# Kernel tuning notes

Hardware: AMD Instinct MI355X
Metric: run time of the kernel (lower is better)

The kernel has to match this reference:

```python
import jax, jax.numpy as jnp
import numpy as np
from jax import lax

B_, T_, C_ = 8, 1024, 768
H_, W_ = 32, 32
N_LAYER, LAYER_ID = 12, 5


def _fancy_init():
    # faithful 'fancy' init from Random_SpatialMix._init_weights
    r01 = LAYER_ID / (N_LAYER - 1)
    r1a0 = 1.0 - LAYER_ID / N_LAYER
    h = np.arange(C_, dtype=np.float64)
    decay = -5 + 8 * (h / (C_ - 1)) ** (0.7 + 1.3 * r01)
    zig = ((np.arange(C_) + 1) % 3 - 1) * 0.5
    first = np.log(0.3) + zig
    xlin = h / C_
    mix_k = xlin ** r1a0
    mix_v = xlin ** r1a0 + 0.3 * r01
    mix_r = xlin ** (0.5 * r1a0)
    f32 = lambda a: jnp.asarray(a, jnp.float32)
    return f32(decay), f32(first), f32(mix_k), f32(mix_v), f32(mix_r)


def setup_inputs() -> dict:
    key = jax.random.key(0)
    ks = jax.random.split(key, 6)
    s = 1.0 / np.sqrt(C_)
    x = jax.random.normal(ks[0], (B_, T_, C_), jnp.float32)
    Wk = jax.random.normal(ks[1], (C_, C_), jnp.float32) * s
    Wv = jax.random.normal(ks[2], (C_, C_), jnp.float32) * s
    Wr = jax.random.normal(ks[3], (C_, C_), jnp.float32) * s
    Wo = jax.random.normal(ks[4], (C_, C_), jnp.float32) * s
    decay, first, mk, mv, mr = _fancy_init()
    perm = jax.random.permutation(ks[5], C_).astype(jnp.int32)
    return dict(x=x, w_key=Wk, w_value=Wv, w_receptance=Wr, w_output=Wo,
                spatial_decay=decay, spatial_first=first,
                mix_k=mk, mix_v=mv, mix_r=mr, perm=perm, H=H_, W=W_)


def _shift2d(a, dh, dw, H, W):
    # zero-padded 2D shift of [B,H,W,g]
    pad = [(0, 0), (max(dh, 0), max(-dh, 0)), (max(dw, 0), max(-dw, 0)), (0, 0)]
    a = jnp.pad(a, pad)
    return a[:, max(-dh, 0):max(-dh, 0) + H, max(-dw, 0):max(-dw, 0) + W, :]


def q_shift(x, H, W, shift_pixel=1, gamma=0.25):
    # VRWKV q_shift: 4 channel groups shifted right/left/down/up, rest copied
    B, T, C = x.shape
    xi = x.reshape(B, H, W, C)
    g = int(C * gamma)
    parts = [
        _shift2d(xi[..., 0:g], 0, shift_pixel, H, W),
        _shift2d(xi[..., g:2 * g], 0, -shift_pixel, H, W),
        _shift2d(xi[..., 2 * g:3 * g], shift_pixel, 0, H, W),
        _shift2d(xi[..., 3 * g:4 * g], -shift_pixel, 0, H, W),
        xi[..., 4 * g:],
    ]
    return jnp.concatenate(parts, axis=-1).reshape(B, T, C)


def wkv(w, u, k, v):
    # RWKV-v4 WKV kernel (numerically stable form). w,u: [C]; k,v: [B,T,C]
    w = -jnp.exp(w)  # kernel applies w = -exp(w)
    B, T, C = k.shape

    def step(carry, kv):
        a, b, p = carry  # each [B,C]
        kt, vt = kv
        q = jnp.maximum(p, u + kt)
        e1 = jnp.exp(p - q)
        e2 = jnp.exp(u + kt - q)
        y = (e1 * a + e2 * vt) / (e1 * b + e2)
        q2 = jnp.maximum(p + w, kt)
        e1 = jnp.exp(p + w - q2)
        e2 = jnp.exp(kt - q2)
        return (e1 * a + e2 * vt, e1 * b + e2, q2), y

    init = (jnp.zeros((B, C), k.dtype), jnp.zeros((B, C), k.dtype),
            jnp.full((B, C), -1e38, k.dtype))
    _, y = lax.scan(step, init, (jnp.moveaxis(k, 1, 0), jnp.moveaxis(v, 1, 0)))
    return jnp.moveaxis(y, 0, 1)


def reference(x, w_key, w_value, w_receptance, w_output,
              spatial_decay, spatial_first, mix_k, mix_v, mix_r, perm, H, W):
    B, T, C = x.shape
    xx = q_shift(x, H, W)
    xk = x * mix_k + xx * (1 - mix_k)
    xv = x * mix_v + xx * (1 - mix_v)
    xr = x * mix_r + xx * (1 - mix_r)
    k = xk @ w_key.T
    v = xv @ w_value.T
    sr = jax.nn.sigmoid(xr @ w_receptance.T)
    # training path: shuffle CHANNEL axis (RevShuffle dim=2), run WKV, reverse
    ks_ = k[:, :, perm]
    vs_ = v[:, :, perm]
    wkv_s = wkv(spatial_decay / T, spatial_first / T, ks_, vs_)
    rev = jnp.zeros_like(perm).at[perm].set(jnp.arange(C, dtype=perm.dtype))
    wkv_out = wkv_s[:, :, rev]
    return (sr * wkv_out) @ w_output.T
```

## Files before the change

kernel.cpp:

```cpp
#include <hip/hip_runtime.h>
#include <hip/hip_bf16.h>
#include <stdint.h>

#define B_N 8
#define T_N 1024
#define C_N 768
#define M_N (B_N*T_N)
#define NCH 32
#define LCH (T_N/NCH)
#define BK32 32
#define KS  (C_N/BK32)

typedef __attribute__((ext_vector_type(4))) float f32x4;
typedef __attribute__((ext_vector_type(8))) short s16x8;
typedef __attribute__((ext_vector_type(4))) unsigned short u16x4;

__device__ __forceinline__ unsigned short f2bf(float f){
  unsigned int u = __float_as_uint(f);
  u += 0x7FFFu + ((u >> 16) & 1u);
  return (unsigned short)(u >> 16);
}
__device__ __forceinline__ float bf2f(unsigned short h){
  return __uint_as_float(((unsigned int)h) << 16);
}

__device__ __forceinline__ void async16(const unsigned short* g, unsigned short* l){
  __builtin_amdgcn_global_load_lds(
      (const __attribute__((address_space(1))) unsigned int*)g,
      (__attribute__((address_space(3))) unsigned int*)l, 16, 0, 0);
}

__global__ __launch_bounds__(256) void prep_mix(
    const float* __restrict__ x,
    const float* __restrict__ Wk, const float* __restrict__ Wv,
    const float* __restrict__ Wr, const float* __restrict__ Wo,
    const int* __restrict__ perm,
    const float* __restrict__ mk, const float* __restrict__ mv, const float* __restrict__ mr,
    unsigned short* __restrict__ Wall, unsigned short* __restrict__ Wop,
    unsigned short* __restrict__ xk, unsigned short* __restrict__ xv,
    unsigned short* __restrict__ xr)
{
  if (blockIdx.x < 2304){
    int idx = blockIdx.x*256 + threadIdx.x;
    int r = idx / C_N, c = idx - r*C_N;
    int pr = perm[r];
    Wall[idx]                     = f2bf(Wk[pr*C_N + c]);
    Wall[idx +   (size_t)C_N*C_N] = f2bf(Wv[pr*C_N + c]);
    Wall[idx + 2*(size_t)C_N*C_N] = f2bf(Wr[pr*C_N + c]);
    Wop[idx] = f2bf(Wo[r*C_N + perm[c]]);
    return;
  }
  int idx = (blockIdx.x - 2304)*256 + threadIdx.x;
  int n  = idx / (C_N/4);
  int c4 = (idx - n*(C_N/4)) * 4;
  int t = n & (T_N-1);
  int h = t >> 5, w = t & 31;
  int grp = c4 / 192;
  int dh = (grp==2) ? -1 : (grp==3) ? 1 : 0;
  int dw = (grp==0) ? -1 : (grp==1) ? 1 : 0;
  int h2 = h + dh, w2 = w + dw;
  bool valid = ((unsigned)h2 < 32u) && ((unsigned)w2 < 32u);
  f32x4 xc = *(const f32x4*)(x + (size_t)n*C_N + c4);
  f32x4 xx = {0.f,0.f,0.f,0.f};
  if (valid) xx = *(const f32x4*)(x + (size_t)(n + dh*32 + dw)*C_N + c4);
  f32x4 vk = *(const f32x4*)(mk + c4);
  f32x4 vv = *(const f32x4*)(mv + c4);
  f32x4 vr = *(const f32x4*)(mr + c4);
  u16x4 ok, ov, orr;
  #pragma unroll
  for (int i=0;i<4;++i){
    float d = xc[i] - xx[i];
    ok[i]  = f2bf(xx[i] + vk[i]*d);
    ov[i]  = f2bf(xx[i] + vv[i]*d);
    orr[i] = f2bf(xx[i] + vr[i]*d);
  }
  *(u16x4*)(xk + (size_t)n*C_N + c4) = ok;
  *(u16x4*)(xv + (size_t)n*C_N + c4) = ov;
  *(u16x4*)(xr + (size_t)n*C_N + c4) = orr;
}

__global__ __launch_bounds__(256, 4) void gemm_kvr(
    const unsigned short* __restrict__ xk, const unsigned short* __restrict__ xv,
    const unsigned short* __restrict__ xr,
    const unsigned short* __restrict__ Wall,
    unsigned short* __restrict__ kb, unsigned short* __restrict__ vb,
    unsigned short* __restrict__ srb)
{
  int flat = blockIdx.y * gridDim.x + blockIdx.x;
  const int xcd = flat & 7, q = flat >> 3;
  const int mb = xcd*8 + (q & 7);
  const int nb = q >> 3;
  const int m0 = mb * 128;
  const int n0 = nb * 128;
  const int z  = nb / 6;
  const unsigned short* A = (z==0)? xk : (z==1)? xv : xr;

  __shared__ union {
    struct { unsigned short As[2][128*BK32]; unsigned short Bs[2][128*BK32]; } s;
    unsigned short ct[64*132];
  } u;
  const int tid = threadIdx.x;
  const int lane = tid & 63, wid = tid >> 6;
  const int wr = wid >> 1, wc = wid & 1;
  f32x4 acc[4][4];
  #pragma unroll
  for (int i=0;i<4;++i)
    #pragma unroll
    for (int j=0;j<4;++j) acc[i][j] = (f32x4){0.f,0.f,0.f,0.f};

  const int sgcol = ((lane & 3) ^ ((lane >> 3) & 3)) * 8;
  const int srow  = lane >> 2;
  const int lr  = lane & 15;
  const int kh  = lane >> 4;
  const int phys = (kh ^ ((lr >> 1) & 3)) * 8;

  auto stage = [&](int buf, int k0){
    #pragma unroll
    for (int i=0;i<2;++i){
      int rbase = i*64 + wid*16;
      async16(&A   [(size_t)(m0 + rbase + srow)*C_N + k0 + sgcol], &u.s.As[buf][rbase*BK32]);
      async16(&Wall[(size_t)(n0 + rbase + srow)*C_N + k0 + sgcol], &u.s.Bs[buf][rbase*BK32]);
    }
  };

  auto compute = [&](int buf){
    s16x8 af[4], bfr[4];
    #pragma unroll
    for (int mi=0;mi<4;++mi) af[mi]  = *(const s16x8*)&u.s.As[buf][(wr*64 + mi*16 + lr)*BK32 + phys];
    #pragma unroll
    for (int ni=0;ni<4;++ni) bfr[ni] = *(const s16x8*)&u.s.Bs[buf][(wc*64 + ni*16 + lr)*BK32 + phys];
    __builtin_amdgcn_s_setprio(1);
    #pragma unroll
    for (int mi=0;mi<4;++mi)
      #pragma unroll
      for (int ni=0;ni<4;++ni)
        acc[mi][ni] = __builtin_amdgcn_mfma_f32_16x16x32_bf16(af[mi], bfr[ni], acc[mi][ni], 0,0,0);
    __builtin_amdgcn_s_setprio(0);
  };

  stage(0, 0);
  #pragma unroll 1
  for (int t = 0; t < KS; ++t){
    if (t + 1 < KS){
      stage((t+1)&1, (t+1)*BK32);
      asm volatile("s_waitcnt vmcnt(4)" ::: "memory");
    } else {
      asm volatile("s_waitcnt vmcnt(0)" ::: "memory");
    }
    __builtin_amdgcn_s_barrier();
    compute(t & 1);
    __builtin_amdgcn_s_barrier();
  }

  unsigned short* dst = (z==0)? kb : (z==1)? vb : srb;
  const int colbase = n0 - z*C_N;
  const int lr4 = (lane>>4)*4, lc = lane & 15;
  #pragma unroll
  for (int p=0;p<2;++p){
    if (p) __builtin_amdgcn_s_barrier();
    if (wr == p){
      #pragma unroll
      for (int mi=0;mi<4;++mi){
        #pragma unroll
        for (int ni=0;ni<4;++ni){
          #pragma unroll
          for (int i=0;i<4;++i){
            int r  = mi*16 + lr4 + i;
            int cc = wc*64 + ni*16 + lc;
            float val = acc[mi][ni][i];
            if (z==2) val = 1.f/(1.f + __expf(-val));
            u.ct[r*132 + cc] = f2bf(val);
          }
        }
      }
    }
    __builtin_amdgcn_s_barrier();
    #pragma unroll
    for (int qq=0;qq<4;++qq){
      int f = (qq*256 + tid)*8;
      int r = f >> 7, cc = f & 127;
      s16x8 v8 = *(const s16x8*)&u.ct[r*132 + cc];
      *(s16x8*)&dst[(size_t)(m0 + p*64 + r)*C_N + colbase + cc] = v8;
    }
  }
}

__global__ __launch_bounds__(256, 4) void gemm_out(
    const unsigned short* __restrict__ A, const unsigned short* __restrict__ Bw,
    float* __restrict__ out)
{
  int flat = blockIdx.y * gridDim.x + blockIdx.x;
  const int xcd = flat & 7, q = flat >> 3;
  const int mb = xcd*8 + (q & 7);
  const int nb = q >> 3;
  const int m0 = mb*128, n0 = nb*128;
  __shared__ __align__(16) unsigned short As[2][128*BK32];
  __shared__ __align__(16) unsigned short Bs[2][128*BK32];
  const int tid = threadIdx.x;
  const int lane = tid & 63, wid = tid >> 6;
  const int wr = wid >> 1, wc = wid & 1;
  f32x4 acc[4][4];
  #pragma unroll
  for (int i=0;i<4;++i)
    #pragma unroll
    for (int j=0;j<4;++j) acc[i][j] = (f32x4){0.f,0.f,0.f,0.f};

  const int sgcol = ((lane & 3) ^ ((lane >> 3) & 3)) * 8;
  const int srow  = lane >> 2;
  const int lr  = lane & 15;
  const int kh  = lane >> 4;
  const int phys = (kh ^ ((lr >> 1) & 3)) * 8;

  auto stage = [&](int buf, int k0){
    #pragma unroll
    for (int i=0;i<2;++i){
      int rbase = i*64 + wid*16;
      async16(&A [(size_t)(m0 + rbase + srow)*C_N + k0 + sgcol], &As[buf][rbase*BK32]);
      async16(&Bw[(size_t)(n0 + rbase + srow)*C_N + k0 + sgcol], &Bs[buf][rbase*BK32]);
    }
  };

  auto compute = [&](int buf){
    s16x8 af[4], bfr[4];
    #pragma unroll
    for (int mi=0;mi<4;++mi) af[mi]  = *(const s16x8*)&As[buf][(wr*64 + mi*16 + lr)*BK32 + phys];
    #pragma unroll
    for (int ni=0;ni<4;++ni) bfr[ni] = *(const s16x8*)&Bs[buf][(wc*64 + ni*16 + lr)*BK32 + phys];
    __builtin_amdgcn_s_setprio(1);
    #pragma unroll
    for (int mi=0;mi<4;++mi)
      #pragma unroll
      for (int ni=0;ni<4;++ni)
        acc[mi][ni] = __builtin_amdgcn_mfma_f32_16x16x32_bf16(af[mi], bfr[ni], acc[mi][ni], 0,0,0);
    __builtin_amdgcn_s_setprio(0);
  };

  stage(0, 0);
  #pragma unroll 1
  for (int t = 0; t < KS; ++t){
    if (t + 1 < KS){
      stage((t+1)&1, (t+1)*BK32);
      asm volatile("s_waitcnt vmcnt(4)" ::: "memory");
    } else {
      asm volatile("s_waitcnt vmcnt(0)" ::: "memory");
    }
    __builtin_amdgcn_s_barrier();
    compute(t & 1);
    __builtin_amdgcn_s_barrier();
  }

  const int lr4 = (lane>>4)*4, lc = lane & 15;
  #pragma unroll
  for (int mi=0;mi<4;++mi)
    #pragma unroll
    for (int ni=0;ni<4;++ni)
      #pragma unroll
      for (int i=0;i<4;++i){
        int m = m0 + wr*64 + mi*16 + lr4 + i;
        int n = n0 + wc*64 + ni*16 + lc;
        out[(size_t)m*C_N + n] = acc[mi][ni][i];
      }
}

__global__ __launch_bounds__(256) void wkv_phase1(
    const unsigned short* __restrict__ kb, const unsigned short* __restrict__ vb,
    const float* __restrict__ decay,
    float* __restrict__ sa, float* __restrict__ sb, float* __restrict__ sp)
{
  int g = blockIdx.x*256 + threadIdx.x;
  int j = g % C_N;
  int cb = g / C_N;
  int b = cb % B_N, c = cb / B_N;
  float w = -__expf(decay[j] * (1.0f/T_N));
  float a = 0.f, bb = 0.f, p = -1e38f;
  size_t base = ((size_t)b*T_N + c*LCH)*C_N + j;
  #pragma unroll 4
  for (int t = 0; t < LCH; ++t){
    size_t o = base + (size_t)t*C_N;
    float kt = bf2f(kb[o]), vt = bf2f(vb[o]);
    float pw = p + w;
    float q2 = fmaxf(pw, kt);
    float e1 = __expf(pw - q2), e2 = __expf(kt - q2);
    a  = e1*a + e2*vt;
    bb = e1*bb + e2;
    p  = q2;
  }
  sa[g] = a; sb[g] = bb; sp[g] = p;
}

__global__ __launch_bounds__(256) void wkv_phase2(
    const float* __restrict__ decay,
    float* __restrict__ sa, float* __restrict__ sb, float* __restrict__ sp)
{
  int g = blockIdx.x*256 + threadIdx.x;
  int j = g % C_N, b = g / C_N;
  float w = -__expf(decay[j] * (1.0f/T_N));
  float wL = w * (float)LCH;
  float a = 0.f, bb = 0.f, p = -1e38f;
  for (int c = 0; c < NCH; ++c){
    size_t idx = ((size_t)c*B_N + b)*C_N + j;
    float la = sa[idx], lb = sb[idx], lp = sp[idx];
    sa[idx] = a; sb[idx] = bb; sp[idx] = p;
    float p1 = p + wL;
    float pn = fmaxf(p1, lp);
    float e1 = __expf(p1 - pn), e2 = __expf(lp - pn);
    a  = e1*a + e2*la;
    bb = e1*bb + e2*lb;
    p  = pn;
  }
}

__global__ __launch_bounds__(256) void wkv_phase3(
    const unsigned short* __restrict__ kb, const unsigned short* __restrict__ vb,
    const unsigned short* __restrict__ srb,
    const float* __restrict__ decay, const float* __restrict__ first,
    const float* __restrict__ sa, const float* __restrict__ sb,
    const float* __restrict__ sp,
    unsigned short* __restrict__ zp)
{
  int g = blockIdx.x*256 + threadIdx.x;
  int j = g % C_N;
  int cb = g / C_N;
  int b = cb % B_N, c = cb / B_N;
  float w = -__expf(decay[j] * (1.0f/T_N));
  float u = first[j] * (1.0f/T_N);
  float a = sa[g], bb = sb[g], p = sp[g];
  size_t base = ((size_t)b*T_N + c*LCH)*C_N + j;
  #pragma unroll 2
  for (int t = 0; t < LCH; ++t){
    size_t o = base + (size_t)t*C_N;
    float kt = bf2f(kb[o]), vt = bf2f(vb[o]);
    float uk = u + kt;
    float q  = fmaxf(p, uk);
    float e1 = __expf(p - q), e2 = __expf(uk - q);
    float y  = __fdividef(e1*a + e2*vt, e1*bb + e2);
    zp[o] = f2bf(bf2f(srb[o]) * y);
    float pw = p + w;
    float q2 = fmaxf(pw, kt);
    float e1b = __expf(pw - q2), e2b = __expf(kt - q2);
    a  = e1b*a + e2b*vt;
    bb = e1b*bb + e2b;
    p  = q2;
  }
}

extern "C" void kernel_launch(void* const* d_in, const int* in_sizes, int n_in,
                              void* d_out, int out_size, void* d_ws, size_t ws_size,
                              hipStream_t stream)
{
  const float* x     = (const float*)d_in[0];
  const float* Wk    = (const float*)d_in[1];
  const float* Wv    = (const float*)d_in[2];
  const float* Wr    = (const float*)d_in[3];
  const float* Wo    = (const float*)d_in[4];
  const float* decay = (const float*)d_in[5];
  const float* first = (const float*)d_in[6];
  const float* mk    = (const float*)d_in[7];
  const float* mv    = (const float*)d_in[8];
  const float* mr    = (const float*)d_in[9];
  const int*   perm  = (const int*)d_in[10];
  float* out = (float*)d_out;

  char* ws = (char*)d_ws;
  size_t off = 0;
  auto alloc = [&](size_t bytes)->char* {
    char* p = ws + off;
    off += (bytes + 255) & ~(size_t)255;
    return p;
  };
  const size_t MC = (size_t)M_N * C_N;
  const size_t CC = (size_t)C_N * C_N;
  const size_t SC = (size_t)NCH * B_N * C_N;
  unsigned short* xk   = (unsigned short*)alloc(MC*2);
  unsigned short* xv   = (unsigned short*)alloc(MC*2);
  unsigned short* xr   = (unsigned short*)alloc(MC*2);
  unsigned short* zp   = (unsigned short*)alloc(MC*2);
  unsigned short* Wall = (unsigned short*)alloc(CC*3*2);
  unsigned short* Wop  = (unsigned short*)alloc(CC*2);
  unsigned short* srb  = (unsigned short*)alloc(MC*2);
  unsigned short* kb   = (unsigned short*)alloc(MC*2);
  unsigned short* vb   = (unsigned short*)alloc(MC*2);
  float* sa  = (float*)alloc(SC*4);
  float* sb  = (float*)alloc(SC*4);
  float* sp  = (float*)alloc(SC*4);

  prep_mix<<<dim3(2304 + 6144), dim3(256), 0, stream>>>(
      x, Wk, Wv, Wr, Wo, perm, mk, mv, mr, Wall, Wop, xk, xv, xr);
  gemm_kvr<<<dim3(M_N/128, 3*C_N/128), dim3(256), 0, stream>>>(
      xk, xv, xr, Wall, kb, vb, srb);
  wkv_phase1<<<dim3(SC/256), dim3(256), 0, stream>>>(kb, vb, decay, sa, sb, sp);
  wkv_phase2<<<dim3(B_N*C_N/256), dim3(256), 0, stream>>>(decay, sa, sb, sp);
  wkv_phase3<<<dim3(SC/256), dim3(256), 0, stream>>>(kb, vb, srb, decay, first,
                                                     sa, sb, sp, zp);
  gemm_out<<<dim3(M_N/128, C_N/128), dim3(256), 0, stream>>>(zp, Wop, out);
}
```

Baseline: 113.7 us.

## Widen kvr GEMM tile to 128x192 and triple-buffer output GEMM

The fused k/v/r GEMM now uses 128x192 tiles, so each wave holds a 4x6 MFMA accumulator block. The grid drops to 768 one-dimensional blocks, with matching changes to staging, waitcnt and the epilogue layout. The output GEMM moves from double to triple buffering with a prefetch distance of two K-steps to hide global load latency. Both kernels lower the occupancy hint to 3 blocks per CU, trading occupancy for more registers and LDS per block.

```diff
diff --git a/kernel.cpp b/kernel.cpp
--- a/kernel.cpp
+++ b/kernel.cpp
@@ -79,34 +79,38 @@
   *(u16x4*)(xr + (size_t)n*C_N + c4) = orr;
 }
 
-__global__ __launch_bounds__(256, 4) void gemm_kvr(
+__global__ __launch_bounds__(256, 3) void gemm_kvr(
     const unsigned short* __restrict__ xk, const unsigned short* __restrict__ xv,
     const unsigned short* __restrict__ xr,
     const unsigned short* __restrict__ Wall,
     unsigned short* __restrict__ kb, unsigned short* __restrict__ vb,
     unsigned short* __restrict__ srb)
 {
-  int flat = blockIdx.y * gridDim.x + blockIdx.x;
+  int flat = blockIdx.x;
   const int xcd = flat & 7, q = flat >> 3;
   const int mb = xcd*8 + (q & 7);
   const int nb = q >> 3;
   const int m0 = mb * 128;
-  const int n0 = nb * 128;
-  const int z  = nb / 6;
+  const int n0 = nb * 192;
+  const int z  = nb >> 2;
   const unsigned short* A = (z==0)? xk : (z==1)? xv : xr;
 
   __shared__ union {
-    struct { unsigned short As[2][128*BK32]; unsigned short Bs[2][128*BK32]; } s;
-    unsigned short ct[64*132];
+    struct {
+      unsigned short As[2][128*BK32];
+      unsigned short Bs[2][192*BK32];
+      unsigned short pad[4096];
+    } s;
+    unsigned short ct[64*200];
   } u;
   const int tid = threadIdx.x;
   const int lane = tid & 63, wid = tid >> 6;
   const int wr = wid >> 1, wc = wid & 1;
-  f32x4 acc[4][4];
+  f32x4 acc[4][6];
   #pragma unroll
   for (int i=0;i<4;++i)
     #pragma unroll
-    for (int j=0;j<4;++j) acc[i][j] = (f32x4){0.f,0.f,0.f,0.f};
+    for (int j=0;j<6;++j) acc[i][j] = (f32x4){0.f,0.f,0.f,0.f};
 
   const int sgcol = ((lane & 3) ^ ((lane >> 3) & 3)) * 8;
   const int srow  = lane >> 2;
@@ -118,22 +122,26 @@
     #pragma unroll
     for (int i=0;i<2;++i){
       int rbase = i*64 + wid*16;
-      async16(&A   [(size_t)(m0 + rbase + srow)*C_N + k0 + sgcol], &u.s.As[buf][rbase*BK32]);
+      async16(&A[(size_t)(m0 + rbase + srow)*C_N + k0 + sgcol], &u.s.As[buf][rbase*BK32]);
+    }
+    #pragma unroll
+    for (int i=0;i<3;++i){
+      int rbase = i*64 + wid*16;
       async16(&Wall[(size_t)(n0 + rbase + srow)*C_N + k0 + sgcol], &u.s.Bs[buf][rbase*BK32]);
     }
   };
 
   auto compute = [&](int buf){
-    s16x8 af[4], bfr[4];
+    s16x8 af[4], bfr[6];
     #pragma unroll
     for (int mi=0;mi<4;++mi) af[mi]  = *(const s16x8*)&u.s.As[buf][(wr*64 + mi*16 + lr)*BK32 + phys];
     #pragma unroll
-    for (int ni=0;ni<4;++ni) bfr[ni] = *(const s16x8*)&u.s.Bs[buf][(wc*64 + ni*16 + lr)*BK32 + phys];
+    for (int ni=0;ni<6;++ni) bfr[ni] = *(const s16x8*)&u.s.Bs[buf][(wc*96 + ni*16 + lr)*BK32 + phys];
     __builtin_amdgcn_s_setprio(1);
     #pragma unroll
     for (int mi=0;mi<4;++mi)
       #pragma unroll
-      for (int ni=0;ni<4;++ni)
+      for (int ni=0;ni<6;++ni)
         acc[mi][ni] = __builtin_amdgcn_mfma_f32_16x16x32_bf16(af[mi], bfr[ni], acc[mi][ni], 0,0,0);
     __builtin_amdgcn_s_setprio(0);
   };
@@ -143,7 +151,7 @@
   for (int t = 0; t < KS; ++t){
     if (t + 1 < KS){
       stage((t+1)&1, (t+1)*BK32);
-      asm volatile("s_waitcnt vmcnt(4)" ::: "memory");
+      asm volatile("s_waitcnt vmcnt(5)" ::: "memory");
     } else {
       asm volatile("s_waitcnt vmcnt(0)" ::: "memory");
     }
@@ -162,30 +170,30 @@
       #pragma unroll
       for (int mi=0;mi<4;++mi){
         #pragma unroll
-        for (int ni=0;ni<4;++ni){
+        for (int ni=0;ni<6;++ni){
           #pragma unroll
           for (int i=0;i<4;++i){
             int r  = mi*16 + lr4 + i;
-            int cc = wc*64 + ni*16 + lc;
+            int cc = wc*96 + ni*16 + lc;
             float val = acc[mi][ni][i];
             if (z==2) val = 1.f/(1.f + __expf(-val));
-            u.ct[r*132 + cc] = f2bf(val);
+            u.ct[r*200 + cc] = f2bf(val);
           }
         }
       }
     }
     __builtin_amdgcn_s_barrier();
     #pragma unroll
-    for (int qq=0;qq<4;++qq){
-      int f = (qq*256 + tid)*8;
-      int r = f >> 7, cc = f & 127;
-      s16x8 v8 = *(const s16x8*)&u.ct[r*132 + cc];
+    for (int qq=0;qq<6;++qq){
+      int ch = qq*256 + tid;
+      int r = ch / 24, cc = (ch - r*24)*8;
+      s16x8 v8 = *(const s16x8*)&u.ct[r*200 + cc];
       *(s16x8*)&dst[(size_t)(m0 + p*64 + r)*C_N + colbase + cc] = v8;
     }
   }
 }
 
-__global__ __launch_bounds__(256, 4) void gemm_out(
+__global__ __launch_bounds__(256, 3) void gemm_out(
     const unsigned short* __restrict__ A, const unsigned short* __restrict__ Bw,
     float* __restrict__ out)
 {
@@ -194,8 +202,8 @@
   const int mb = xcd*8 + (q & 7);
   const int nb = q >> 3;
   const int m0 = mb*128, n0 = nb*128;
-  __shared__ __align__(16) unsigned short As[2][128*BK32];
-  __shared__ __align__(16) unsigned short Bs[2][128*BK32];
+  __shared__ __align__(16) unsigned short As[3][128*BK32];
+  __shared__ __align__(16) unsigned short Bs[3][128*BK32];
   const int tid = threadIdx.x;
   const int lane = tid & 63, wid = tid >> 6;
   const int wr = wid >> 1, wc = wid & 1;
@@ -236,16 +244,15 @@
   };
 
   stage(0, 0);
+  stage(1, BK32);
   #pragma unroll 1
   for (int t = 0; t < KS; ++t){
-    if (t + 1 < KS){
-      stage((t+1)&1, (t+1)*BK32);
-      asm volatile("s_waitcnt vmcnt(4)" ::: "memory");
-    } else {
-      asm volatile("s_waitcnt vmcnt(0)" ::: "memory");
-    }
+    if (t + 2 < KS) stage((t+2)%3, (t+2)*BK32);
+    if (t + 2 < KS)      asm volatile("s_waitcnt vmcnt(8)" ::: "memory");
+    else if (t + 1 < KS) asm volatile("s_waitcnt vmcnt(4)" ::: "memory");
+    else                 asm volatile("s_waitcnt vmcnt(0)" ::: "memory");
     __builtin_amdgcn_s_barrier();
-    compute(t & 1);
+    compute(t%3);
     __builtin_amdgcn_s_barrier();
   }
 
@@ -386,7 +393,7 @@
 
   prep_mix<<<dim3(2304 + 6144), dim3(256), 0, stream>>>(
       x, Wk, Wv, Wr, Wo, perm, mk, mv, mr, Wall, Wop, xk, xv, xr);
-  gemm_kvr<<<dim3(M_N/128, 3*C_N/128), dim3(256), 0, stream>>>(
+  gemm_kvr<<<dim3(768), dim3(256), 0, stream>>>(
       xk, xv, xr, Wall, kb, vb, srb);
   wkv_phase1<<<dim3(SC/256), dim3(256), 0, stream>>>(kb, vb, decay, sa, sb, sp);
   wkv_phase2<<<dim3(B_N*C_N/256), dim3(256), 0, stream>>>(decay, sa, sb, sp);
```

Result: faster. 108.8 us (-4.3%).
